# Kernel tuning notes

Measured on AMD Instinct MI355X. Metric: run time of the kernel, lower is better.

Reference implementation:

```python
import jax, jax.numpy as jnp
import numpy as np

B, CENT, IN_CH, OUT_CH, NDIAG = 32, 2, 8, 16, 64


def setup_inputs() -> dict:
    key = jax.random.key(0)
    k1, k2, k3 = jax.random.split(key, 3)
    D = jax.random.normal(k1, (B, CENT, IN_CH, NDIAG), dtype=jnp.float32)
    C = jax.random.normal(k2, (CENT, IN_CH, NDIAG, NDIAG), dtype=jnp.float32)
    # weight is constrained non-negative (NonNeg constraint + tf.abs in build)
    w = jax.random.uniform(k3, (NDIAG, CENT, IN_CH, OUT_CH), dtype=jnp.float32)
    return {"D": D, "C": C, "w": w}


def reference(D, C, w):
    # Faithful math: u from SVD of C (s, v unused in the original call);
    # spd = sum_{c,n} u @ diag(einsum('bcnd,dcno', D, w)) @ u^T
    w = jnp.abs(w)  # mirrors tf.abs(self.w) in build
    u, _, _ = jnp.linalg.svd(C, full_matrices=False)  # (c, n, d, d)
    svec = jnp.einsum('bcnd,dcno->bcnod', D, w)        # diagonal entries, no diag() blow-up
    # u diag(svec) u^T, fused: avoids materializing (b,c,n,o,d,d) diag matrix
    spd = jnp.einsum('cnid,bcnod,cnjd->boij', u, svec, u)  # (b, o, d, d)
    return spd
```

## Files before the change

### kernel.cpp

```cpp
#include <hip/hip_runtime.h>
#include <math.h>


#define NSWEEP 8
#define NROUND (NSWEEP * 63)

__device__ __forceinline__ float bper(int paddr, float v) {
    return __int_as_float(__builtin_amdgcn_ds_bpermute(paddr, __float_as_int(v)));
}

__device__ __forceinline__ float pdot32(const float (&a)[32], const float (&b)[32]) {
    float d0 = 0.f, d1 = 0.f, d2 = 0.f, d3 = 0.f;
    #pragma unroll
    for (int i = 0; i < 32; i += 4) {
        d0 = fmaf(a[i],     b[i],     d0);
        d1 = fmaf(a[i + 1], b[i + 1], d1);
        d2 = fmaf(a[i + 2], b[i + 2], d2);
        d3 = fmaf(a[i + 3], b[i + 3], d3);
    }
    return (d0 + d1) + (d2 + d3);
}

__device__ __forceinline__ void round_body(
    float (&g)[32], float (&tin)[32], float (&tout)[32],
    float& nrm, float& gam, float& pn, int& m,
    const int lane, const int wv, float (&pex)[2][2][64],
    const int par_next, const bool last)
{
    const int partner = lane ^ m;
    const bool is_p = lane < partner;

    const float diff = pn - nrm;
    const float num  = is_p ? diff : -diff;
    const float zeta = num * 0.5f * __builtin_amdgcn_rcpf(gam);
    const float t0   = copysignf(1.f, zeta) *
                       __builtin_amdgcn_rcpf(fabsf(zeta) + sqrtf(fmaf(zeta, zeta, 1.f)));
    const float t    = (fabsf(gam) > 1e-30f) ? t0 : 0.f;
    const float c    = __builtin_amdgcn_rsqf(fmaf(t, t, 1.f));
    const float s    = t * c;
    const float sa   = is_p ? -s : s;
    const float ta   = is_p ? -t : t;
    nrm = fmaf(ta, gam, nrm);

    m = (m == 63) ? 1 : m + 1;

    if (last) {
        #pragma unroll
        for (int i = 0; i < 32; i++) g[i] = fmaf(c, g[i], sa * tin[i]);
        return;
    }

    const int paddr = (lane ^ m) << 2;
    #pragma unroll
    for (int i = 0; i < 32; i++) {
        g[i]    = fmaf(c, g[i], sa * tin[i]);
        tout[i] = bper(paddr, g[i]);
    }
    pn = bper(paddr, nrm);

    const float part = pdot32(g, tout);
    pex[par_next][wv][lane] = part;
    __syncthreads();
    gam = part + pex[par_next][wv ^ 1][lane];
}

__global__ __launch_bounds__(128, 1) void eig_kernel(const float* __restrict__ C,
                                                     float* __restrict__ ut) {
    __shared__ float pex[2][2][64];
    __shared__ float sn[64];

    const int mat  = blockIdx.x;
    const int tid  = threadIdx.x;
    const int wv   = tid >> 6;
    const int lane = tid & 63;
    const int row0 = wv << 5;
    const float* Cm = C + mat * 4096;

    float g[32];
    #pragma unroll
    for (int i = 0; i < 32; i++) g[i] = Cm[(row0 + i) * 64 + lane];

    float nrm;
    {
        const float part = pdot32(g, g);
        pex[1][wv][lane] = part;
        __syncthreads();
        nrm = part + pex[1][wv ^ 1][lane];
    }

    float tA[32], tB[32];
    float gam, pn;
    int m = 1;

    {
        const int paddr = (lane ^ 1) << 2;
        #pragma unroll
        for (int i = 0; i < 32; i++) tA[i] = bper(paddr, g[i]);
        pn = bper(paddr, nrm);
        const float part = pdot32(g, tA);
        pex[0][wv][lane] = part;
        __syncthreads();
        gam = part + pex[0][wv ^ 1][lane];
    }

    for (int r = 0; r < NROUND; r += 2) {
        round_body(g, tA, tB, nrm, gam, pn, m, lane, wv, pex, 1, false);
        round_body(g, tB, tA, nrm, gam, pn, m, lane, wv, pex, 0, r + 2 >= NROUND);
    }

    {
        const float part = pdot32(g, g);
        __syncthreads();
        pex[0][wv][lane] = part;
        __syncthreads();
        nrm = part + pex[0][wv ^ 1][lane];
    }

    if (wv == 0) sn[lane] = nrm;
    __syncthreads();
    int rank = 0;
    #pragma unroll 8
    for (int e = 0; e < 64; e++) {
        const float ne = sn[e];
        rank += (ne > nrm) || (ne == nrm && e < lane);
    }

    const float inv = __builtin_amdgcn_rsqf(fmaxf(nrm, 1e-30f));
    float* dst = ut + (mat * 64 + rank) * 64 + row0;
    #pragma unroll
    for (int i = 0; i < 32; i++) dst[i] = g[i] * inv;
}

__global__ __launch_bounds__(256) void spd_kernel(const float* __restrict__ D,
                                                  const float* __restrict__ w,
                                                  const float* __restrict__ ut,
                                                  float* __restrict__ out) {
    __shared__ __align__(16) float U[64][64];
    __shared__ float t[64];

    const int bid = blockIdx.x;
    const int b = bid >> 4, o = bid & 15;
    const int tid = threadIdx.x;
    const int ti = tid & 15, tj = tid >> 4;

    float acc[4][4] = {{0.f, 0.f, 0.f, 0.f}, {0.f, 0.f, 0.f, 0.f},
                       {0.f, 0.f, 0.f, 0.f}, {0.f, 0.f, 0.f, 0.f}};

    for (int cn = 0; cn < 16; cn++) {
        __syncthreads();
        const float4* src = (const float4*)(ut + cn * 4096);
        float4* dstU = (float4*)(&U[0][0]);
        #pragma unroll
        for (int idx = tid; idx < 1024; idx += 256) dstU[idx] = src[idx];
        if (tid < 64) {
            int d = tid;
            float dv = D[(b * 16 + cn) * 64 + d];
            float wv = fabsf(w[(d * 16 + cn) * 16 + o]);
            t[d] = dv * wv;
        }
        __syncthreads();

        #pragma unroll 4
        for (int d = 0; d < 64; d++) {
            float td = t[d];
            float4 uiv = *(const float4*)(&U[d][ti * 4]);
            float4 ujv = *(const float4*)(&U[d][tj * 4]);
            float si0 = td * uiv.x, si1 = td * uiv.y, si2 = td * uiv.z, si3 = td * uiv.w;
            acc[0][0] += si0 * ujv.x; acc[0][1] += si0 * ujv.y; acc[0][2] += si0 * ujv.z; acc[0][3] += si0 * ujv.w;
            acc[1][0] += si1 * ujv.x; acc[1][1] += si1 * ujv.y; acc[1][2] += si1 * ujv.z; acc[1][3] += si1 * ujv.w;
            acc[2][0] += si2 * ujv.x; acc[2][1] += si2 * ujv.y; acc[2][2] += si2 * ujv.z; acc[2][3] += si2 * ujv.w;
            acc[3][0] += si3 * ujv.x; acc[3][1] += si3 * ujv.y; acc[3][2] += si3 * ujv.z; acc[3][3] += si3 * ujv.w;
        }
    }

    float* obase = out + (size_t)bid * 4096;
    #pragma unroll
    for (int k = 0; k < 4; k++) {
        float4 v = make_float4(acc[k][0], acc[k][1], acc[k][2], acc[k][3]);
        *(float4*)(&obase[(ti * 4 + k) * 64 + tj * 4]) = v;
    }
}

extern "C" void kernel_launch(void* const* d_in, const int* in_sizes, int n_in,
                              void* d_out, int out_size, void* d_ws, size_t ws_size,
                              hipStream_t stream) {
    const float* D = (const float*)d_in[0];
    const float* C = (const float*)d_in[1];
    const float* w = (const float*)d_in[2];
    float* out = (float*)d_out;
    float* ut  = (float*)d_ws;

    hipLaunchKernelGGL(eig_kernel, dim3(16), dim3(128), 0, stream, C, ut);
    hipLaunchKernelGGL(spd_kernel, dim3(512), dim3(256), 0, stream, D, w, ut, out);
}
```

Before: 327.4 us.

## Split Jacobi eigen kernel rows across four waves and simplify round loop

The one-sided Jacobi eigensolver now runs with 256 threads (four wavefronts) per matrix, so each thread holds 16 rows instead of 32. The per-round work per thread is halved. The previous pipelined round structure, which carried the partner column and overlapped the next round's dot product with the rotation, is replaced by a plain loop that exchanges, reduces, then rotates. That loop needs two block barriers per round instead of one, and the latency-hiding overlap is lost.

```diff
diff --git a/kernel.cpp b/kernel.cpp
--- a/kernel.cpp
+++ b/kernel.cpp
@@ -9,10 +9,10 @@
     return __int_as_float(__builtin_amdgcn_ds_bpermute(paddr, __float_as_int(v)));
 }
 
-__device__ __forceinline__ float pdot32(const float (&a)[32], const float (&b)[32]) {
+__device__ __forceinline__ float pdot16(const float (&a)[16], const float (&b)[16]) {
     float d0 = 0.f, d1 = 0.f, d2 = 0.f, d3 = 0.f;
     #pragma unroll
-    for (int i = 0; i < 32; i += 4) {
+    for (int i = 0; i < 16; i += 4) {
         d0 = fmaf(a[i],     b[i],     d0);
         d1 = fmaf(a[i + 1], b[i + 1], d1);
         d2 = fmaf(a[i + 2], b[i + 2], d2);
@@ -21,99 +21,70 @@
     return (d0 + d1) + (d2 + d3);
 }
 
-__device__ __forceinline__ void round_body(
-    float (&g)[32], float (&tin)[32], float (&tout)[32],
-    float& nrm, float& gam, float& pn, int& m,
-    const int lane, const int wv, float (&pex)[2][2][64],
-    const int par_next, const bool last)
-{
-    const int partner = lane ^ m;
-    const bool is_p = lane < partner;
-
-    const float diff = pn - nrm;
-    const float num  = is_p ? diff : -diff;
-    const float zeta = num * 0.5f * __builtin_amdgcn_rcpf(gam);
-    const float t0   = copysignf(1.f, zeta) *
-                       __builtin_amdgcn_rcpf(fabsf(zeta) + sqrtf(fmaf(zeta, zeta, 1.f)));
-    const float t    = (fabsf(gam) > 1e-30f) ? t0 : 0.f;
-    const float c    = __builtin_amdgcn_rsqf(fmaf(t, t, 1.f));
-    const float s    = t * c;
-    const float sa   = is_p ? -s : s;
-    const float ta   = is_p ? -t : t;
-    nrm = fmaf(ta, gam, nrm);
-
-    m = (m == 63) ? 1 : m + 1;
-
-    if (last) {
-        #pragma unroll
-        for (int i = 0; i < 32; i++) g[i] = fmaf(c, g[i], sa * tin[i]);
-        return;
-    }
-
-    const int paddr = (lane ^ m) << 2;
-    #pragma unroll
-    for (int i = 0; i < 32; i++) {
-        g[i]    = fmaf(c, g[i], sa * tin[i]);
-        tout[i] = bper(paddr, g[i]);
-    }
-    pn = bper(paddr, nrm);
-
-    const float part = pdot32(g, tout);
-    pex[par_next][wv][lane] = part;
-    __syncthreads();
-    gam = part + pex[par_next][wv ^ 1][lane];
-}
-
-__global__ __launch_bounds__(128, 1) void eig_kernel(const float* __restrict__ C,
+__global__ __launch_bounds__(256, 1) void eig_kernel(const float* __restrict__ C,
                                                      float* __restrict__ ut) {
-    __shared__ float pex[2][2][64];
+    __shared__ float pex[4][64];
     __shared__ float sn[64];
 
     const int mat  = blockIdx.x;
     const int tid  = threadIdx.x;
     const int wv   = tid >> 6;
     const int lane = tid & 63;
-    const int row0 = wv << 5;
+    const int row0 = wv << 4;
     const float* Cm = C + mat * 4096;
 
-    float g[32];
+    float g[16];
     #pragma unroll
-    for (int i = 0; i < 32; i++) g[i] = Cm[(row0 + i) * 64 + lane];
+    for (int i = 0; i < 16; i++) g[i] = Cm[(row0 + i) * 64 + lane];
 
     float nrm;
     {
-        const float part = pdot32(g, g);
-        pex[1][wv][lane] = part;
+        pex[wv][lane] = pdot16(g, g);
         __syncthreads();
-        nrm = part + pex[1][wv ^ 1][lane];
+        nrm = (pex[0][lane] + pex[1][lane]) + (pex[2][lane] + pex[3][lane]);
+        __syncthreads();
     }
 
-    float tA[32], tB[32];
-    float gam, pn;
     int m = 1;
+    for (int r = 0; r < NROUND; ++r) {
+        const int partner = lane ^ m;
+        const int paddr   = partner << 2;
 
-    {
-        const int paddr = (lane ^ 1) << 2;
+        float tmp[16];
         #pragma unroll
-        for (int i = 0; i < 32; i++) tA[i] = bper(paddr, g[i]);
-        pn = bper(paddr, nrm);
-        const float part = pdot32(g, tA);
-        pex[0][wv][lane] = part;
+        for (int i = 0; i < 16; i++) tmp[i] = bper(paddr, g[i]);
+        const float pn = bper(paddr, nrm);
+
+        const float part = pdot16(g, tmp);
+        pex[wv][lane] = part;
         __syncthreads();
-        gam = part + pex[0][wv ^ 1][lane];
-    }
+        const float gam = (pex[0][lane] + pex[1][lane]) + (pex[2][lane] + pex[3][lane]);
+        __syncthreads();
 
-    for (int r = 0; r < NROUND; r += 2) {
-        round_body(g, tA, tB, nrm, gam, pn, m, lane, wv, pex, 1, false);
-        round_body(g, tB, tA, nrm, gam, pn, m, lane, wv, pex, 0, r + 2 >= NROUND);
+        const bool  is_p = lane < partner;
+        const float diff = pn - nrm;
+        const float num  = is_p ? diff : -diff;
+        const float zeta = num * 0.5f * __builtin_amdgcn_rcpf(gam);
+        const float t0   = copysignf(1.f, zeta) *
+                           __builtin_amdgcn_rcpf(fabsf(zeta) + sqrtf(fmaf(zeta, zeta, 1.f)));
+        const float t    = (fabsf(gam) > 1e-30f) ? t0 : 0.f;
+        const float c    = __builtin_amdgcn_rsqf(fmaf(t, t, 1.f));
+        const float s    = t * c;
+        const float sa   = is_p ? -s : s;
+        const float ta   = is_p ? -t : t;
+
+        #pragma unroll
+        for (int i = 0; i < 16; i++) g[i] = fmaf(c, g[i], sa * tmp[i]);
+        nrm = fmaf(ta, gam, nrm);
+
+        m = (m == 63) ? 1 : m + 1;
     }
 
     {
-        const float part = pdot32(g, g);
+        const float part = pdot16(g, g);
+        pex[wv][lane] = part;
         __syncthreads();
-        pex[0][wv][lane] = part;
-        __syncthreads();
-        nrm = part + pex[0][wv ^ 1][lane];
+        nrm = (pex[0][lane] + pex[1][lane]) + (pex[2][lane] + pex[3][lane]);
     }
 
     if (wv == 0) sn[lane] = nrm;
@@ -128,7 +99,7 @@
     const float inv = __builtin_amdgcn_rsqf(fmaxf(nrm, 1e-30f));
     float* dst = ut + (mat * 64 + rank) * 64 + row0;
     #pragma unroll
-    for (int i = 0; i < 32; i++) dst[i] = g[i] * inv;
+    for (int i = 0; i < 16; i++) dst[i] = g[i] * inv;
 }
 
 __global__ __launch_bounds__(256) void spd_kernel(const float* __restrict__ D,
@@ -190,6 +161,6 @@
     float* out = (float*)d_out;
     float* ut  = (float*)d_ws;
 
-    hipLaunchKernelGGL(eig_kernel, dim3(16), dim3(128), 0, stream, C, ut);
+    hipLaunchKernelGGL(eig_kernel, dim3(16), dim3(256), 0, stream, C, ut);
     hipLaunchKernelGGL(spd_kernel, dim3(512), dim3(256), 0, stream, D, w, ut, out);
 }
```

After: 319.6 us. 2.4% less time.
